# Kernel tuning notes

Hardware: AMD Instinct MI355X
Metric: run time of the kernel (lower is better)

## Reference

```python
import jax, jax.numpy as jnp
import numpy as np

N_CHANNEL = 64
N_BAND = 5
N_CLASS = 2
B = 64
K = 2 * N_CHANNEL  # nodes covered by the fully-connected edge_index


def _w(key, shape):
    fan_in = shape[0] if len(shape) == 2 else int(np.prod(shape[1:]))
    return (jax.random.normal(key, shape, jnp.float32) / np.float32(np.sqrt(fan_in)))


def setup_inputs() -> dict:
    key = jax.random.key(0)
    ks = jax.random.split(key, 22)
    d = {}
    d['x1'] = jax.random.normal(ks[0], (B, K, N_BAND), jnp.float32)
    d['x2'] = jax.random.normal(ks[1], (B, K, K), jnp.float32)
    # GCNConv params (weights stored (in, out); PyG applies linear then aggregates, bias after)
    d['gcn1_w'] = _w(ks[2], (N_BAND, 2 * N_BAND))
    d['gcn1_b'] = 0.01 * jax.random.normal(ks[3], (2 * N_BAND,), jnp.float32)
    d['gcn2_w'] = _w(ks[4], (2 * N_BAND, 1))
    d['gcn2_b'] = 0.01 * jax.random.normal(ks[5], (1,), jnp.float32)
    d['fcg_w'] = _w(ks[6], (K, K))
    d['fcg_b'] = 0.01 * jax.random.normal(ks[7], (K,), jnp.float32)
    d['conv1_w'] = _w(ks[8], (16, 1, 3, 3))   # OIHW
    d['conv1_b'] = 0.01 * jax.random.normal(ks[9], (16,), jnp.float32)
    d['conv2_w'] = _w(ks[10], (16, 16, 3, 3))
    d['conv2_b'] = 0.01 * jax.random.normal(ks[11], (16,), jnp.float32)
    d['fcc_w'] = _w(ks[12], (16 * K * K, K))
    d['fcc_b'] = 0.01 * jax.random.normal(ks[13], (K,), jnp.float32)
    d['fc1_w'] = _w(ks[14], (4 * N_CHANNEL, 2 * N_CHANNEL))
    d['fc1_b'] = 0.01 * jax.random.normal(ks[15], (2 * N_CHANNEL,), jnp.float32)
    d['fc2_w'] = _w(ks[16], (2 * N_CHANNEL, N_CHANNEL))
    d['fc2_b'] = 0.01 * jax.random.normal(ks[17], (N_CHANNEL,), jnp.float32)
    d['fc3_w'] = _w(ks[18], (N_CHANNEL, N_CLASS))
    d['fc3_b'] = 0.01 * jax.random.normal(ks[19], (N_CLASS,), jnp.float32)
    return d


def _gcn(x, W, b):
    # Faithful to original: edge_index is fully connected over the FIRST K rows only.
    # With default self-loops, normalized adjacency over rows [0,K) is (1/K)*ones(K,K)
    # (all degrees = K); every other row has only its self-loop (degree 1 -> identity).
    y = x @ W                                   # (B*N, out)
    y = y.at[:K].set(jnp.mean(y[:K], axis=0))   # broadcast mean over first K rows
    return y + b


def _conv(x, w, b):
    y = jax.lax.conv_general_dilated(x, w, (1, 1), 'SAME',
                                     dimension_numbers=('NCHW', 'OIHW', 'NCHW'))
    return jax.nn.relu(y + b[None, :, None, None])


def reference(x1, x2, gcn1_w, gcn1_b, gcn2_w, gcn2_b, fcg_w, fcg_b,
              conv1_w, conv1_b, conv2_w, conv2_b, fcc_w, fcc_b,
              fc1_w, fc1_b, fc2_w, fc2_b, fc3_w, fc3_b):
    Bn, N, Feat = x1.shape
    # GNN branch (dropout is identity in eval mode)
    h = x1.reshape(Bn * N, Feat)
    h = jax.nn.relu(_gcn(h, gcn1_w, gcn1_b))
    h = jax.nn.relu(_gcn(h, gcn2_w, gcn2_b))
    h = h.reshape(Bn, -1)                       # (B, 2*n_channel)
    g = jax.nn.relu(h @ fcg_w + fcg_b)
    # CNN branch
    c = x2[:, None]                             # (B,1,H,W)
    c = _conv(c, conv1_w, conv1_b)
    c = _conv(c, conv2_w, conv2_b)
    c = c.reshape(Bn, -1)                       # channel-major flatten, same as torch .view
    c = jax.nn.relu(c @ fcc_w + fcc_b)
    # Fusion MLP
    x = jnp.concatenate([c, g], axis=1)
    x = jax.nn.relu(x @ fc1_w + fc1_b)
    x = jax.nn.relu(x @ fc2_w + fc2_b)
    return jax.nn.sigmoid(x @ fc3_w + fc3_b)
```

## Files before the change

### kernel.cpp

```cpp
#include <hip/hip_runtime.h>
#include <hip/hip_bf16.h>


#define NROWS   8192
#define IMG     16384
#define FCC_K   262144
#define FCC_BLOCKS 512
#define FCC_KRANGE 512
#define FCC_CHUNK 64
#define FCC_NCHUNK 8

typedef __attribute__((ext_vector_type(8))) short bf16x8;
typedef __attribute__((ext_vector_type(4))) float f32x4;
typedef __attribute__((ext_vector_type(4))) unsigned short us4;
typedef __attribute__((ext_vector_type(8))) unsigned short us8;

__device__ __forceinline__ unsigned short f2bf(float f) {
    unsigned u = __float_as_uint(f);
    unsigned r = (u + 0x7FFFu + ((u >> 16) & 1u)) >> 16;
    return (unsigned short)r;
}

__device__ __forceinline__ int fcc_swz64(int col, int k) {
    return col*64 + (k ^ ((((col >> 2) ^ col) & 7) << 3));
}

__global__ __launch_bounds__(256) void conv12_kernel(
    const float* __restrict__ x2,
    const float* __restrict__ w1,
    const float* __restrict__ b1,
    const float* __restrict__ w2,
    const float* __restrict__ b2,
    unsigned short* __restrict__ c2bf)
{
    __shared__ float sx2[8][130];
    __shared__ unsigned short sin[6*130*16];
    __shared__ unsigned short sB[5*512];
    __shared__ float sw1[144], sb1v[16];

    int tid = threadIdx.x;
    int blk = blockIdx.x;
    int b   = blk >> 5;
    int R0  = (blk & 31) * 4;

    if (tid < 144) sw1[tid] = w1[tid];
    if (tid < 16)  sb1v[tid] = b1[tid];

    for (int idx = tid; idx < 2560; idx += 256) {
        int q   = idx >> 9;
        int rem = idx & 511;
        int l   = rem >> 3;
        int e   = rem & 7;
        int k   = (l >> 4) * 8 + e;
        int oc  = l & 15;
        int ic  = k & 15;
        int dd  = 2*q + (k >> 4);
        unsigned short bits = 0;
        if (dd < 9) bits = f2bf(w2[oc*144 + ic*9 + dd]);
        sB[idx] = bits;
    }
    if (tid < 192) {
        int rr = tid >> 5, rem = tid & 31;
        int cc = (rem < 16) ? 0 : 129;
        sin[(rr*130 + cc)*16 + (rem & 15)] = 0;
    }
    {
        const float* xb = x2 + (size_t)b * IMG;
        for (int idx = tid; idx < 8*130; idx += 256) {
            int rr = idx / 130, cc = idx - rr*130;
            int ri = R0 - 2 + rr, gj = cc - 1;
            float v = 0.f;
            if (ri >= 0 && ri < 128 && gj >= 0 && gj < 128)
                v = xb[ri*128 + gj];
            sx2[rr][cc] = v;
        }
    }
    __syncthreads();

    for (int p = tid; p < 768; p += 256) {
        int rr = p >> 7;
        int cc = p & 127;
        int ri1 = R0 - 1 + rr;
        bool valid = (ri1 >= 0 && ri1 < 128);
        float in9[3][3];
        #pragma unroll
        for (int di = 0; di < 3; ++di)
          #pragma unroll
          for (int dj = 0; dj < 3; ++dj)
              in9[di][dj] = sx2[rr + di][cc + dj];
        us8 o0, o1;
        #pragma unroll
        for (int oc = 0; oc < 16; ++oc) {
            float acc = sb1v[oc];
            #pragma unroll
            for (int di = 0; di < 3; ++di)
              #pragma unroll
              for (int dj = 0; dj < 3; ++dj)
                  acc += in9[di][dj] * sw1[oc*9 + di*3 + dj];
            unsigned short bits = valid ? f2bf(fmaxf(acc, 0.f)) : (unsigned short)0;
            if (oc < 8) o0[oc] = bits; else o1[oc - 8] = bits;
        }
        unsigned short* dst = &sin[(rr*130 + cc + 1)*16];
        *reinterpret_cast<us8*>(dst)     = o0;
        *reinterpret_cast<us8*>(dst + 8) = o1;
    }
    __syncthreads();

    int lane = tid & 63;
    int wv   = tid >> 6;
    int ln   = lane & 15;
    int g    = lane >> 4;
    int ghalf = g & 1;

    int aoff[5];
    #pragma unroll
    for (int q = 0; q < 5; ++q) {
        int dd = 2*q + (g >> 1);
        if (dd > 8) dd = 8;
        int di = dd / 3, dj = dd % 3;
        aoff[q] = ((wv + di)*130 + ln + dj)*16 + ghalf*8;
    }

    bf16x8 bf[5];
    #pragma unroll
    for (int q = 0; q < 5; ++q)
        bf[q] = *reinterpret_cast<const bf16x8*>(&sB[q*512 + lane*8]);

    float bias_oc = b2[ln];
    int r = R0 + wv;
    unsigned short* outbase = c2bf + ((size_t)b*16 + ln)*IMG + r*128;

    #pragma unroll
    for (int t = 0; t < 8; ++t) {
        f32x4 acc = {0.f, 0.f, 0.f, 0.f};
        #pragma unroll
        for (int q = 0; q < 5; ++q) {
            bf16x8 a = *reinterpret_cast<const bf16x8*>(&sin[aoff[q] + t*256]);
            acc = __builtin_amdgcn_mfma_f32_16x16x32_bf16(a, bf[q], acc, 0, 0, 0);
        }
        int pc = t*16 + g*4;
        us4 pk;
        #pragma unroll
        for (int reg = 0; reg < 4; ++reg)
            pk[reg] = f2bf(fmaxf(acc[reg] + bias_oc, 0.f));
        *reinterpret_cast<us4*>(&outbase[pc]) = pk;
    }
}

__global__ __launch_bounds__(256, 2) void fcc_mfma(
    const unsigned short* __restrict__ c2bf,
    const float* __restrict__ W,
    float* __restrict__ partials)
{
    __shared__ unsigned short sWt[2][FCC_CHUNK*128];

    int tid  = threadIdx.x;
    int blk  = blockIdx.x;
    int k0   = blk * FCC_KRANGE;
    int lane = tid & 63, wv = tid >> 6;
    int ln   = lane & 15, g = lane >> 4;
    int q    = tid & 31;
    int kO   = tid >> 5;

    f32x4 acc[8];
    #pragma unroll
    for (int j = 0; j < 8; ++j) acc[j] = (f32x4){0.f,0.f,0.f,0.f};

    const float* Wb = W + (size_t)k0 * 128;
    const unsigned short* arow = c2bf + (size_t)(16*wv + ln)*FCC_K + k0 + g*8;
    int col0 = q*4;

    float4 rows[8];
    bf16x8 afc0, afc1, afn0, afn1;

    #pragma unroll
    for (int r = 0; r < 8; ++r)
        rows[r] = *reinterpret_cast<const float4*>(
            Wb + (size_t)(kO*8 + r)*128 + col0);
    afc0 = *reinterpret_cast<const bf16x8*>(arow);
    afc1 = *reinterpret_cast<const bf16x8*>(arow + 32);
    {
        us8 vc0, vc1, vc2, vc3;
        #pragma unroll
        for (int r = 0; r < 8; ++r) {
            vc0[r] = f2bf(rows[r].x); vc1[r] = f2bf(rows[r].y);
            vc2[r] = f2bf(rows[r].z); vc3[r] = f2bf(rows[r].w);
        }
        *reinterpret_cast<us8*>(&sWt[0][fcc_swz64(col0+0, kO*8)]) = vc0;
        *reinterpret_cast<us8*>(&sWt[0][fcc_swz64(col0+1, kO*8)]) = vc1;
        *reinterpret_cast<us8*>(&sWt[0][fcc_swz64(col0+2, kO*8)]) = vc2;
        *reinterpret_cast<us8*>(&sWt[0][fcc_swz64(col0+3, kO*8)]) = vc3;
    }
    __syncthreads();

    for (int ci = 0; ci < FCC_NCHUNK; ++ci) {
        const unsigned short* bufC = &sWt[ci & 1][0];
        if (ci < FCC_NCHUNK-1) {
            const float* Wc = Wb + (size_t)(ci + 1) * FCC_CHUNK * 128;
            #pragma unroll
            for (int r = 0; r < 8; ++r)
                rows[r] = *reinterpret_cast<const float4*>(
                    Wc + (size_t)(kO*8 + r)*128 + col0);
            afn0 = *reinterpret_cast<const bf16x8*>(arow + (ci+1)*FCC_CHUNK);
            afn1 = *reinterpret_cast<const bf16x8*>(arow + (ci+1)*FCC_CHUNK + 32);
        }
        #pragma unroll
        for (int j = 0; j < 8; ++j) {
            bf16x8 bfrag = *reinterpret_cast<const bf16x8*>(
                &bufC[fcc_swz64(j*16 + ln, g*8)]);
            acc[j] = __builtin_amdgcn_mfma_f32_16x16x32_bf16(afc0, bfrag, acc[j], 0, 0, 0);
        }
        #pragma unroll
        for (int j = 0; j < 8; ++j) {
            bf16x8 bfrag = *reinterpret_cast<const bf16x8*>(
                &bufC[fcc_swz64(j*16 + ln, 32 + g*8)]);
            acc[j] = __builtin_amdgcn_mfma_f32_16x16x32_bf16(afc1, bfrag, acc[j], 0, 0, 0);
        }
        __syncthreads();
        if (ci < FCC_NCHUNK-1) {
            unsigned short* bufN = &sWt[(ci + 1) & 1][0];
            us8 vc0, vc1, vc2, vc3;
            #pragma unroll
            for (int r = 0; r < 8; ++r) {
                vc0[r] = f2bf(rows[r].x); vc1[r] = f2bf(rows[r].y);
                vc2[r] = f2bf(rows[r].z); vc3[r] = f2bf(rows[r].w);
            }
            *reinterpret_cast<us8*>(&bufN[fcc_swz64(col0+0, kO*8)]) = vc0;
            *reinterpret_cast<us8*>(&bufN[fcc_swz64(col0+1, kO*8)]) = vc1;
            *reinterpret_cast<us8*>(&bufN[fcc_swz64(col0+2, kO*8)]) = vc2;
            *reinterpret_cast<us8*>(&bufN[fcc_swz64(col0+3, kO*8)]) = vc3;
            afc0 = afn0; afc1 = afn1;
        }
        __syncthreads();
    }

    float* p = partials + (size_t)blk * 8192;
    #pragma unroll
    for (int j = 0; j < 8; ++j)
      #pragma unroll
      for (int reg = 0; reg < 4; ++reg) {
          int m = 16*wv + g*4 + reg;
          p[m*128 + j*16 + ln] = acc[j][reg];
      }
}

__global__ __launch_bounds__(512) void head_kernel(
    const float* __restrict__ partials,
    const float* __restrict__ fccb,
    const float* __restrict__ x1,
    const float* __restrict__ gW1,
    const float* __restrict__ gb1,
    const float* __restrict__ gW2,
    const float* __restrict__ gb2,
    const float* __restrict__ fcgW,
    const float* __restrict__ fcgb,
    const float* __restrict__ w1, const float* __restrict__ bb1,
    const float* __restrict__ w2, const float* __restrict__ bb2,
    const float* __restrict__ w3, const float* __restrict__ bb3,
    float* __restrict__ out)
{
    __shared__ float sred[4][128];
    __shared__ float sx[256], sh[128], s2[64], sh2[128];
    __shared__ float sW1[50], sb1s[10], sW2s[10], smean[10];
    __shared__ float sy1[128][10];
    int b = blockIdx.x, t = threadIdx.x;
    int o = t & 127, pr = t >> 7;

    {
        const float* pb = partials + (size_t)pr*8192 + (size_t)b*128 + o;
        float s = 0.f;
        #pragma unroll 8
        for (int p = 0; p < FCC_BLOCKS/4; ++p) s += pb[(size_t)p*4*8192];
        sred[pr][o] = s;
    }
    if (t < 50) sW1[t] = gW1[t];
    if (t >= 64 && t < 74) { sb1s[t-64] = gb1[t-64]; sW2s[t-64] = gW2[t-64]; }
    __syncthreads();

    if (t < 128)
        sx[t] = fmaxf(sred[0][t] + sred[1][t] + sred[2][t] + sred[3][t]
                      + fccb[t], 0.f);

    float y[10];
    if (t < 128) {
        int r = b*128 + t;
        float x[5];
        #pragma unroll
        for (int f = 0; f < 5; ++f) x[f] = x1[r*5 + f];
        #pragma unroll
        for (int oo = 0; oo < 10; ++oo) {
            float a = 0.f;
            #pragma unroll
            for (int f = 0; f < 5; ++f) a += x[f] * sW1[f*10 + oo];
            y[oo] = a;
        }
    }
    if (b == 0) {
        if (t < 128) {
            #pragma unroll
            for (int oo = 0; oo < 10; ++oo) sy1[t][oo] = y[oo];
        }
        __syncthreads();
        if (t < 10) {
            float s = 0.f;
            for (int rr = 0; rr < 128; ++rr) s += sy1[rr][t];
            smean[t] = fmaxf(s * (1.f/128.f) + sb1s[t], 0.f);
        }
        __syncthreads();
    }
    if (t < 128) {
        float h1row[10];
        if (b == 0) {
            #pragma unroll
            for (int oo = 0; oo < 10; ++oo) h1row[oo] = smean[oo];
        } else {
            #pragma unroll
            for (int oo = 0; oo < 10; ++oo) h1row[oo] = fmaxf(y[oo] + sb1s[oo], 0.f);
        }
        float y2 = 0.f;
        #pragma unroll
        for (int oo = 0; oo < 10; ++oo) y2 += h1row[oo] * sW2s[oo];
        sh2[t] = fmaxf(y2 + gb2[0], 0.f);
    }
    __syncthreads();

    if (t < 128) {
        float acc = fcgb[t];
        #pragma unroll 8
        for (int k = 0; k < 128; ++k) acc += sh2[k] * fcgW[k*128 + t];
        sx[128 + t] = fmaxf(acc, 0.f);
    }
    __syncthreads();

    if (t < 128) {
        float acc = bb1[t];
        for (int k = 0; k < 256; ++k) acc += sx[k] * w1[k*128 + t];
        sh[t] = fmaxf(acc, 0.f);
    }
    __syncthreads();
    if (t < 64) {
        float acc = bb2[t];
        for (int k = 0; k < 128; ++k) acc += sh[k] * w2[k*64 + t];
        s2[t] = fmaxf(acc, 0.f);
    }
    __syncthreads();
    if (t < 2) {
        float acc = bb3[t];
        for (int k = 0; k < 64; ++k) acc += s2[k] * w3[k*2 + t];
        out[b*2 + t] = 1.f / (1.f + __expf(-acc));
    }
}

extern "C" void kernel_launch(void* const* d_in, const int* in_sizes, int n_in,
                              void* d_out, int out_size, void* d_ws, size_t ws_size,
                              hipStream_t stream)
{
    const float* x1      = (const float*)d_in[0];
    const float* x2      = (const float*)d_in[1];
    const float* gcn1_w  = (const float*)d_in[2];
    const float* gcn1_b  = (const float*)d_in[3];
    const float* gcn2_w  = (const float*)d_in[4];
    const float* gcn2_b  = (const float*)d_in[5];
    const float* fcg_w   = (const float*)d_in[6];
    const float* fcg_b   = (const float*)d_in[7];
    const float* conv1_w = (const float*)d_in[8];
    const float* conv1_b = (const float*)d_in[9];
    const float* conv2_w = (const float*)d_in[10];
    const float* conv2_b = (const float*)d_in[11];
    const float* fcc_w   = (const float*)d_in[12];
    const float* fcc_b   = (const float*)d_in[13];
    const float* fc1_w   = (const float*)d_in[14];
    const float* fc1_b   = (const float*)d_in[15];
    const float* fc2_w   = (const float*)d_in[16];
    const float* fc2_b   = (const float*)d_in[17];
    const float* fc3_w   = (const float*)d_in[18];
    const float* fc3_b   = (const float*)d_in[19];
    float* out = (float*)d_out;

    unsigned short* c2bf = (unsigned short*)d_ws;
    float* partials = (float*)(c2bf + 16777216);

    conv12_kernel<<<2048, 256, 0, stream>>>(x2, conv1_w, conv1_b,
                                            conv2_w, conv2_b, c2bf);
    fcc_mfma<<<FCC_BLOCKS, 256, 0, stream>>>(c2bf, fcc_w, partials);
    head_kernel<<<64, 512, 0, stream>>>(partials, fcc_b,
                                        x1, gcn1_w, gcn1_b, gcn2_w, gcn2_b,
                                        fcg_w, fcg_b,
                                        fc1_w, fc1_b, fc2_w, fc2_b,
                                        fc3_w, fc3_b, out);
}
```

Before: 90.25 us.

## Deepen fcc weight prefetch, preload all A fragments, store partials as bf16

The fcc MFMA kernel now loads all sixteen A-fragments for its K range up front and keeps two register stages of weight rows in flight. The chunk loop is fully unrolled over ping-pong shared buffers, so global weight loads run two chunks ahead of compute. Split-K partials are written as bf16 instead of fp32, halving partial traffic for the head kernel's reduction. The cost is higher register pressure under the 2-blocks-per-CU launch bound, extra barriers, and bf16 rounding error accumulated across 512 partial sums.

```diff
diff --git a/kernel.cpp b/kernel.cpp
--- a/kernel.cpp
+++ b/kernel.cpp
@@ -2,13 +2,11 @@
 #include <hip/hip_bf16.h>
 
 
-#define NROWS   8192
 #define IMG     16384
 #define FCC_K   262144
 #define FCC_BLOCKS 512
 #define FCC_KRANGE 512
 #define FCC_CHUNK 64
-#define FCC_NCHUNK 8
 
 typedef __attribute__((ext_vector_type(8))) short bf16x8;
 typedef __attribute__((ext_vector_type(4))) float f32x4;
@@ -19,6 +17,10 @@
     unsigned u = __float_as_uint(f);
     unsigned r = (u + 0x7FFFu + ((u >> 16) & 1u)) >> 16;
     return (unsigned short)r;
+}
+__device__ __forceinline__ float bf2f(unsigned short b) {
+    unsigned u = ((unsigned)b) << 16;
+    return __uint_as_float(u);
 }
 
 __device__ __forceinline__ int fcc_swz64(int col, int k) {
@@ -147,10 +149,49 @@
     }
 }
 
+#define STAGE_LOAD(ROWS, CI)                                                  \
+    {                                                                         \
+        const float* Wc_ = Wb + (size_t)(CI) * FCC_CHUNK * 128;               \
+        _Pragma("unroll")                                                     \
+        for (int r = 0; r < 8; ++r)                                           \
+            ROWS[r] = *reinterpret_cast<const float4*>(                       \
+                Wc_ + (size_t)(kO*8 + r)*128 + col0);                         \
+    }
+
+#define STAGE_WRITE(ROWS, BUF)                                                \
+    {                                                                         \
+        us8 vc0, vc1, vc2, vc3;                                               \
+        _Pragma("unroll")                                                     \
+        for (int r = 0; r < 8; ++r) {                                         \
+            vc0[r] = f2bf(ROWS[r].x); vc1[r] = f2bf(ROWS[r].y);               \
+            vc2[r] = f2bf(ROWS[r].z); vc3[r] = f2bf(ROWS[r].w);               \
+        }                                                                     \
+        *reinterpret_cast<us8*>(&(BUF)[fcc_swz64(col0+0, kO*8)]) = vc0;       \
+        *reinterpret_cast<us8*>(&(BUF)[fcc_swz64(col0+1, kO*8)]) = vc1;       \
+        *reinterpret_cast<us8*>(&(BUF)[fcc_swz64(col0+2, kO*8)]) = vc2;       \
+        *reinterpret_cast<us8*>(&(BUF)[fcc_swz64(col0+3, kO*8)]) = vc3;       \
+    }
+
+#define COMPUTE_CHUNK(BUF, AF0, AF1)                                          \
+    {                                                                         \
+        _Pragma("unroll")                                                     \
+        for (int j = 0; j < 8; ++j) {                                         \
+            bf16x8 bfrag = *reinterpret_cast<const bf16x8*>(                  \
+                &(BUF)[fcc_swz64(j*16 + ln, g*8)]);                           \
+            acc[j] = __builtin_amdgcn_mfma_f32_16x16x32_bf16(AF0, bfrag, acc[j], 0, 0, 0); \
+        }                                                                     \
+        _Pragma("unroll")                                                     \
+        for (int j = 0; j < 8; ++j) {                                         \
+            bf16x8 bfrag = *reinterpret_cast<const bf16x8*>(                  \
+                &(BUF)[fcc_swz64(j*16 + ln, 32 + g*8)]);                      \
+            acc[j] = __builtin_amdgcn_mfma_f32_16x16x32_bf16(AF1, bfrag, acc[j], 0, 0, 0); \
+        }                                                                     \
+    }
+
 __global__ __launch_bounds__(256, 2) void fcc_mfma(
     const unsigned short* __restrict__ c2bf,
     const float* __restrict__ W,
-    float* __restrict__ partials)
+    unsigned short* __restrict__ partials)
 {
     __shared__ unsigned short sWt[2][FCC_CHUNK*128];
 
@@ -161,6 +202,7 @@
     int ln   = lane & 15, g = lane >> 4;
     int q    = tid & 31;
     int kO   = tid >> 5;
+    int col0 = q*4;
 
     f32x4 acc[8];
     #pragma unroll
@@ -168,92 +210,51 @@
 
     const float* Wb = W + (size_t)k0 * 128;
     const unsigned short* arow = c2bf + (size_t)(16*wv + ln)*FCC_K + k0 + g*8;
-    int col0 = q*4;
-
-    float4 rows[8];
-    bf16x8 afc0, afc1, afn0, afn1;
-
-    #pragma unroll
-    for (int r = 0; r < 8; ++r)
-        rows[r] = *reinterpret_cast<const float4*>(
-            Wb + (size_t)(kO*8 + r)*128 + col0);
-    afc0 = *reinterpret_cast<const bf16x8*>(arow);
-    afc1 = *reinterpret_cast<const bf16x8*>(arow + 32);
-    {
-        us8 vc0, vc1, vc2, vc3;
-        #pragma unroll
-        for (int r = 0; r < 8; ++r) {
-            vc0[r] = f2bf(rows[r].x); vc1[r] = f2bf(rows[r].y);
-            vc2[r] = f2bf(rows[r].z); vc3[r] = f2bf(rows[r].w);
-        }
-        *reinterpret_cast<us8*>(&sWt[0][fcc_swz64(col0+0, kO*8)]) = vc0;
-        *reinterpret_cast<us8*>(&sWt[0][fcc_swz64(col0+1, kO*8)]) = vc1;
-        *reinterpret_cast<us8*>(&sWt[0][fcc_swz64(col0+2, kO*8)]) = vc2;
-        *reinterpret_cast<us8*>(&sWt[0][fcc_swz64(col0+3, kO*8)]) = vc3;
-    }
-    __syncthreads();
-
-    for (int ci = 0; ci < FCC_NCHUNK; ++ci) {
-        const unsigned short* bufC = &sWt[ci & 1][0];
-        if (ci < FCC_NCHUNK-1) {
-            const float* Wc = Wb + (size_t)(ci + 1) * FCC_CHUNK * 128;
-            #pragma unroll
-            for (int r = 0; r < 8; ++r)
-                rows[r] = *reinterpret_cast<const float4*>(
-                    Wc + (size_t)(kO*8 + r)*128 + col0);
-            afn0 = *reinterpret_cast<const bf16x8*>(arow + (ci+1)*FCC_CHUNK);
-            afn1 = *reinterpret_cast<const bf16x8*>(arow + (ci+1)*FCC_CHUNK + 32);
-        }
-        #pragma unroll
-        for (int j = 0; j < 8; ++j) {
-            bf16x8 bfrag = *reinterpret_cast<const bf16x8*>(
-                &bufC[fcc_swz64(j*16 + ln, g*8)]);
-            acc[j] = __builtin_amdgcn_mfma_f32_16x16x32_bf16(afc0, bfrag, acc[j], 0, 0, 0);
-        }
-        #pragma unroll
-        for (int j = 0; j < 8; ++j) {
-            bf16x8 bfrag = *reinterpret_cast<const bf16x8*>(
-                &bufC[fcc_swz64(j*16 + ln, 32 + g*8)]);
-            acc[j] = __builtin_amdgcn_mfma_f32_16x16x32_bf16(afc1, bfrag, acc[j], 0, 0, 0);
-        }
-        __syncthreads();
-        if (ci < FCC_NCHUNK-1) {
-            unsigned short* bufN = &sWt[(ci + 1) & 1][0];
-            us8 vc0, vc1, vc2, vc3;
-            #pragma unroll
-            for (int r = 0; r < 8; ++r) {
-                vc0[r] = f2bf(rows[r].x); vc1[r] = f2bf(rows[r].y);
-                vc2[r] = f2bf(rows[r].z); vc3[r] = f2bf(rows[r].w);
-            }
-            *reinterpret_cast<us8*>(&bufN[fcc_swz64(col0+0, kO*8)]) = vc0;
-            *reinterpret_cast<us8*>(&bufN[fcc_swz64(col0+1, kO*8)]) = vc1;
-            *reinterpret_cast<us8*>(&bufN[fcc_swz64(col0+2, kO*8)]) = vc2;
-            *reinterpret_cast<us8*>(&bufN[fcc_swz64(col0+3, kO*8)]) = vc3;
-            afc0 = afn0; afc1 = afn1;
-        }
-        __syncthreads();
-    }
-
-    float* p = partials + (size_t)blk * 8192;
+
+    bf16x8 af[16];
+    #pragma unroll
+    for (int i = 0; i < 16; ++i)
+        af[i] = *reinterpret_cast<const bf16x8*>(arow + i*32);
+
+    float4 rows_a[8], rows_b[8];
+    STAGE_LOAD(rows_a, 0)
+    STAGE_LOAD(rows_b, 1)
+    STAGE_WRITE(rows_a, sWt[0])
+    __syncthreads();
+
+    #pragma unroll
+    for (int d = 0; d < 4; ++d) {
+        if (d < 3) STAGE_LOAD(rows_a, 2*d + 2)
+        COMPUTE_CHUNK(sWt[0], af[4*d + 0], af[4*d + 1])
+        __syncthreads();
+        STAGE_WRITE(rows_b, sWt[1])
+        __syncthreads();
+        if (d < 3) STAGE_LOAD(rows_b, 2*d + 3)
+        COMPUTE_CHUNK(sWt[1], af[4*d + 2], af[4*d + 3])
+        __syncthreads();
+        if (d < 3) {
+            STAGE_WRITE(rows_a, sWt[0])
+            __syncthreads();
+        }
+    }
+
+    unsigned short* p = partials + (size_t)blk * 8192;
     #pragma unroll
     for (int j = 0; j < 8; ++j)
       #pragma unroll
       for (int reg = 0; reg < 4; ++reg) {
           int m = 16*wv + g*4 + reg;
-          p[m*128 + j*16 + ln] = acc[j][reg];
+          p[m*128 + j*16 + ln] = f2bf(acc[j][reg]);
       }
 }
 
 __global__ __launch_bounds__(512) void head_kernel(
-    const float* __restrict__ partials,
+    const unsigned short* __restrict__ partials,
     const float* __restrict__ fccb,
     const float* __restrict__ x1,
-    const float* __restrict__ gW1,
-    const float* __restrict__ gb1,
-    const float* __restrict__ gW2,
-    const float* __restrict__ gb2,
-    const float* __restrict__ fcgW,
-    const float* __restrict__ fcgb,
+    const float* __restrict__ gW1, const float* __restrict__ gb1,
+    const float* __restrict__ gW2, const float* __restrict__ gb2,
+    const float* __restrict__ fcgW, const float* __restrict__ fcgb,
     const float* __restrict__ w1, const float* __restrict__ bb1,
     const float* __restrict__ w2, const float* __restrict__ bb2,
     const float* __restrict__ w3, const float* __restrict__ bb3,
@@ -267,10 +268,10 @@
     int o = t & 127, pr = t >> 7;
 
     {
-        const float* pb = partials + (size_t)pr*8192 + (size_t)b*128 + o;
+        const unsigned short* pb = partials + (size_t)pr*8192 + (size_t)b*128 + o;
         float s = 0.f;
         #pragma unroll 8
-        for (int p = 0; p < FCC_BLOCKS/4; ++p) s += pb[(size_t)p*4*8192];
+        for (int p = 0; p < FCC_BLOCKS/4; ++p) s += bf2f(pb[(size_t)p*4*8192]);
         sred[pr][o] = s;
     }
     if (t < 50) sW1[t] = gW1[t];
@@ -377,8 +378,8 @@
     const float* fc3_b   = (const float*)d_in[19];
     float* out = (float*)d_out;
 
-    unsigned short* c2bf = (unsigned short*)d_ws;
-    float* partials = (float*)(c2bf + 16777216);
+    unsigned short* c2bf     = (unsigned short*)d_ws;
+    unsigned short* partials = c2bf + 16777216;
 
     conv12_kernel<<<2048, 256, 0, stream>>>(x2, conv1_w, conv1_b,
                                             conv2_w, conv2_b, c2bf);
```

After: 90.79 us. Within noise of the previous version (+0.6%).
